# Performance work log

Hardware: AMD Instinct MI355X
Metric: run time of the kernel (lower is better)

## Reference

```python
import jax, jax.numpy as jnp
import numpy as np

L, B, S, D, H = 3, 2, 2048, 512, 8
HD = D // H
EPS = 1e-5
NEG = -1e9

def setup_inputs() -> dict:
    key = jax.random.key(0)
    ks = jax.random.split(key, 12)
    sc = 1.0 / np.sqrt(D)
    w = lambda k, shape: (jax.random.normal(k, shape, jnp.float32) * sc)
    return {
        'x': jax.random.normal(ks[0], (B, S, D), jnp.float32),
        'mask': jax.random.randint(ks[1], (B, S), 0, 2).astype(jnp.int32),
        'Wp': w(ks[2], (L, D, D)), 'bp': jnp.zeros((L, D), jnp.float32),
        'gamma': jnp.ones((L, D), jnp.float32), 'beta_ln': jnp.zeros((L, D), jnp.float32),
        'Wq': w(ks[3], (L, D, D)), 'bq': jnp.zeros((L, D), jnp.float32),
        'Wk': w(ks[4], (L, D, D)), 'bk': jnp.zeros((L, D), jnp.float32),
        'Wv': w(ks[5], (L, D, D)), 'bv': jnp.zeros((L, D), jnp.float32),
        'Wo': w(ks[6], (L, D, D)), 'bo': jnp.zeros((L, D), jnp.float32),
        'Wout': w(ks[7], (L * D, D)), 'bout': jnp.zeros((D,), jnp.float32),
    }

def reference(x, mask, Wp, bp, gamma, beta_ln, Wq, bq, Wk, bk, Wv, bv, Wo, bo, Wout, bout):
    # per-level input projection: [L,B,S,D]
    xl = jnp.einsum('bsd,lde->lbse', x, Wp) + bp[:, None, None, :]
    # LayerNorm over last dim
    m = xl.mean(-1, keepdims=True)
    v = xl.var(-1, keepdims=True)
    xn = (xl - m) / jnp.sqrt(v + EPS) * gamma[:, None, None, :] + beta_ln[:, None, None, :]
    proj = lambda W, b: (jnp.einsum('lbsd,lde->lbse', xn, W) + b[:, None, None, :]).reshape(L, B, S, H, HD)
    Q, K, V = proj(Wq, bq), proj(Wk, bk), proj(Wv, bv)
    scores = jnp.einsum('lbqhd,lbkhd->lbhqk', Q, K) / np.sqrt(HD).astype(np.float32)
    scores = jnp.where(mask[None, :, None, None, :] == 0, NEG, scores)
    attn = jax.nn.softmax(scores, axis=-1)  # dropout is identity in eval
    attended = jnp.einsum('lbhqk,lbkhd->lbqhd', attn, V).reshape(L, B, S, D)
    lev = jnp.einsum('lbsd,lde->lbse', attended, Wo) + bo[:, None, None, :]  # [L,B,S,D]
    combined = jnp.moveaxis(lev, 0, 2).reshape(B, S, L * D)  # concat levels on last dim
    return combined @ Wout + bout
```

## Files before the change

kernel.cpp:

```cpp
#include <hip/hip_runtime.h>

typedef unsigned short ushort_t;
typedef __attribute__((ext_vector_type(8))) short bf16x8;
typedef __attribute__((ext_vector_type(4))) float f32x4;
typedef __attribute__((ext_vector_type(4))) unsigned int u32x4;
typedef __attribute__((ext_vector_type(2))) unsigned int u32x2;

#define DI static __device__ __forceinline__

DI ushort_t f2bf(float f){
  unsigned u = __builtin_bit_cast(unsigned, f);
  u += 0x7fffu + ((u >> 16) & 1u);
  return (ushort_t)(u >> 16);
}
DI float bf2f(ushort_t h){ unsigned u = ((unsigned)h) << 16; return __builtin_bit_cast(float, u); }

DI unsigned cvt_pk_bf16(float a, float b){
  unsigned r;
  asm("v_cvt_pk_bf16_f32 %0, %1, %2" : "=v"(r) : "v"(a), "v"(b));
  return r;
}

DI float exp2_fast(float x){
  float r;
  asm("v_exp_f32 %0, %1" : "=v"(r) : "v"(x));
  return r;
}

DI void gload_lds16(const void* g, void* l){
  __builtin_amdgcn_global_load_lds((const __attribute__((address_space(1))) void*)g,
                                   (__attribute__((address_space(3))) void*)l, 16, 0, 0);
}

#define CLOG2E 0.18033688011112042f


__global__ __launch_bounds__(256)
void prep_kernel(const float* __restrict__ x, const float* __restrict__ Wo,
                 const float* __restrict__ Wp, const float* __restrict__ Wq,
                 const float* __restrict__ Wk, const float* __restrict__ Wv,
                 const float* __restrict__ Wout,
                 const float* __restrict__ bq, const float* __restrict__ bk,
                 const float* __restrict__ bv, const int* __restrict__ mask,
                 const float* __restrict__ bo, const float* __restrict__ bout,
                 ushort_t* __restrict__ xb, ushort_t* __restrict__ WoB,
                 ushort_t* __restrict__ WpT, ushort_t* __restrict__ WqkvT,
                 ushort_t* __restrict__ WoutT, float* __restrict__ bqkv,
                 ushort_t* __restrict__ mones, ushort_t* __restrict__ mzero,
                 float* __restrict__ zbias, float* __restrict__ bcomb){
  __shared__ float tile[32][33];
  const int bid = blockIdx.x, tid = threadIdx.x;

  auto do_cast = [&](const float* in, ushort_t* out, int i, int n4){
    if (i >= n4) return;
    float4 v = ((const float4*)in)[i];
    ushort_t r0 = f2bf(v.x), r1 = f2bf(v.y), r2 = f2bf(v.z), r3 = f2bf(v.w);
    ushort_t* o = out + (size_t)i * 4;
    o[0] = r0; o[1] = r1; o[2] = r2; o[3] = r3;
  };
  auto do_transpose = [&](const float* src, ushort_t* dst, int R, int C,
                          int bx, int by, float scale){
    int c0 = bx * 32, r0 = by * 32;
    int tx = tid & 31, ty = tid >> 5;
    #pragma unroll
    for (int p = 0; p < 4; ++p)
      tile[ty + p * 8][tx] = src[(size_t)(r0 + ty + p * 8) * C + c0 + tx];
    __syncthreads();
    #pragma unroll
    for (int p = 0; p < 4; ++p){
      int rr = ty + p * 8;
      dst[(size_t)(c0 + rr) * R + r0 + tx] = f2bf(tile[tx][rr] * scale);
    }
  };

  if (bid < 2048){
    do_cast(x, xb, bid * 256 + tid, 524288);
  } else if (bid < 2816){
    do_cast(Wo, WoB, (bid - 2048) * 256 + tid, 196608);
  } else if (bid < 5888){
    int idx = bid - 2816;
    int w = idx / 768, r = idx % 768;
    int zz = r >> 8, t = r & 255;
    int bx = t & 15, by = t >> 4;
    if (w == 0)      do_transpose(Wp + zz * 262144, WpT + zz * 262144, 512, 512, bx, by, 1.0f);
    else if (w == 1) do_transpose(Wq + zz * 262144, WqkvT + (size_t)zz * 786432, 512, 512, bx, by, CLOG2E);
    else if (w == 2) do_transpose(Wk + zz * 262144, WqkvT + 262144 + (size_t)zz * 786432, 512, 512, bx, by, 1.0f);
    else             do_transpose(Wv + zz * 262144, WqkvT + 524288 + (size_t)zz * 786432, 512, 512, bx, by, 1.0f);
  } else if (bid < 6656){
    int t = bid - 5888;
    do_transpose(Wout, WoutT, 1536, 512, t & 15, t >> 4, 1.0f);
  } else if (bid < 6674){
    int i = (bid - 6656) * 256 + tid;
    if (i < 4608){
      int l = i / 1536, j = i % 1536;
      float v = (j < 512) ? bq[l * 512 + j] * CLOG2E
              : (j < 1024 ? bk[l * 512 + j - 512] : bv[l * 512 + j - 1024]);
      bqkv[i] = v;
    }
  } else if (bid < 6690){
    int i = (bid - 6674) * 256 + tid;
    if (i < 4096){
      int mv = mask[i];
      mones[i] = mv ? (ushort_t)0x3F80 : (ushort_t)0;
      mzero[i] = mv ? (ushort_t)0xFFFF : (ushort_t)0;
    }
    if (i < 512) zbias[i] = 0.f;
  } else {
    int wid = tid >> 6, lane = tid & 63;
    int n = (bid - 6690) * 4 + wid;
    float s = 0.f;
    #pragma unroll
    for (int it = 0; it < 24; ++it){
      int k = it * 64 + lane;
      s += bo[k] * Wout[(size_t)k * 512 + n];
    }
    #pragma unroll
    for (int off = 32; off; off >>= 1) s += __shfl_xor(s, off);
    if (lane == 0) bcomb[n] = s + bout[n];
  }
}


template<int BN>
DI void gemm_mainloop(ushort_t* __restrict__ smem,
                      const ushort_t* __restrict__ A, const ushort_t* __restrict__ Bt,
                      int K, int lda, int ldb, int n0, int m0,
                      f32x4 (&acc)[4][BN / 32]){
  constexpr int NB = BN / 32;
  ushort_t* const As = smem;
  ushort_t* const Bs = smem + 128 * 64;
  const int tid = threadIdx.x, wid = tid >> 6, lane = tid & 63;
  const int wr = wid >> 1, wc = wid & 1, lr = lane & 15, lk = lane >> 4;

  for (int k0 = 0; k0 < K; k0 += 64){
    #pragma unroll
    for (int i = 0; i < 4; ++i){
      const int chunk = i * 256 + wid * 64 + lane;
      const int row = chunk >> 3, cc = chunk & 7;
      gload_lds16(A + (size_t)(m0 + row) * lda + (k0 + cc * 8), &As[(i * 256 + wid * 64) * 8]);
    }
    #pragma unroll
    for (int i = 0; i < NB; ++i){
      const int chunk = i * 256 + wid * 64 + lane;
      const int row = chunk >> 3, cc = chunk & 7;
      gload_lds16(Bt + (size_t)(n0 + row) * ldb + (k0 + cc * 8), &Bs[(i * 256 + wid * 64) * 8]);
    }
    __syncthreads();
    bf16x8 af[4][2], bfr[NB][2];
    #pragma unroll
    for (int m = 0; m < 4; ++m){
      af[m][0] = *(const bf16x8*)&As[(wr * 64 + m * 16 + lr) * 64 + lk * 8];
      af[m][1] = *(const bf16x8*)&As[(wr * 64 + m * 16 + lr) * 64 + 32 + lk * 8];
    }
    #pragma unroll
    for (int n = 0; n < NB; ++n){
      bfr[n][0] = *(const bf16x8*)&Bs[(wc * (BN / 2) + n * 16 + lr) * 64 + lk * 8];
      bfr[n][1] = *(const bf16x8*)&Bs[(wc * (BN / 2) + n * 16 + lr) * 64 + 32 + lk * 8];
    }
    #pragma unroll
    for (int m = 0; m < 4; ++m)
      #pragma unroll
      for (int n = 0; n < NB; ++n){
        acc[m][n] = __builtin_amdgcn_mfma_f32_16x16x32_bf16(af[m][0], bfr[n][0], acc[m][n], 0, 0, 0);
        acc[m][n] = __builtin_amdgcn_mfma_f32_16x16x32_bf16(af[m][1], bfr[n][1], acc[m][n], 0, 0, 0);
      }
    __syncthreads();
  }
}

template<int BF16OUT, int BN>
DI void gemm_store(const f32x4 (&acc)[4][BN / 32], const float* __restrict__ bias,
                   void* __restrict__ Cv, int n0, int m0, int ldc){
  constexpr int NB = BN / 32;
  const int tid = threadIdx.x, wid = tid >> 6, lane = tid & 63;
  const int wr = wid >> 1, wc = wid & 1, lr = lane & 15, lk = lane >> 4;
  #pragma unroll
  for (int n = 0; n < NB; ++n){
    const int col = n0 + wc * (BN / 2) + n * 16 + lr;
    const float bv = bias[col];
    #pragma unroll
    for (int m = 0; m < 4; ++m){
      const int row0 = m0 + wr * 64 + m * 16 + lk * 4;
      #pragma unroll
      for (int j = 0; j < 4; ++j){
        const float v = acc[m][n][j] + bv;
        const size_t idx = (size_t)(row0 + j) * ldc + col;
        if (BF16OUT) ((ushort_t*)Cv)[idx] = f2bf(v);
        else         ((float*)Cv)[idx] = v;
      }
    }
  }
}


template<int BF16OUT, int BN, int VT>
__global__ __launch_bounds__(256)
void gemm_bt(const ushort_t* __restrict__ A, const ushort_t* __restrict__ Bt,
             const float* __restrict__ bias, void* __restrict__ Cv,
             int M, int N, int K, int lda, int ldb, int ldc,
             long long sA, long long sB, long long sC, long long sBias,
             ushort_t* __restrict__ VtG, const ushort_t* __restrict__ mzero){
  constexpr int NB = BN / 32;
  __shared__ ushort_t smem[128 * 64 + BN * 64];
  const int z = blockIdx.z;
  A += (size_t)z * sA; Bt += (size_t)z * sB; bias += (size_t)z * sBias;
  const int n0 = blockIdx.x * BN, m0 = blockIdx.y * 128;
  const int tid = threadIdx.x, wid = tid >> 6, lane = tid & 63;
  const int wr = wid >> 1, wc = wid & 1, lr = lane & 15, lk = lane >> 4;

  f32x4 acc[4][NB] = {};
  gemm_mainloop<BN>(smem, A, Bt, K, lda, ldb, n0, m0, acc);

  if (VT && n0 >= 1024){
    #pragma unroll
    for (int n = 0; n < NB; ++n){
      const int c = wc * (BN / 2) + n * 16 + lr;
      const float bv = bias[n0 + c];
      #pragma unroll
      for (int m = 0; m < 4; ++m){
        const int r0 = wr * 64 + m * 16 + lk * 4;
        u32x2 pk;
        pk[0] = cvt_pk_bf16(acc[m][n][0] + bv, acc[m][n][1] + bv);
        pk[1] = cvt_pk_bf16(acc[m][n][2] + bv, acc[m][n][3] + bv);
        *(u32x2*)&smem[c * 128 + (r0 ^ ((c & 7) << 3))] = pk;
      }
    }
    __syncthreads();
    const int d_ = tid >> 1;
    const int gcol = n0 + d_;
    const int hh = (gcol - 1024) >> 6, dd = gcol & 63;
    const int b_ = m0 >> 11, s0g = m0 & 2047;
    ushort_t* dst = VtG + (((size_t)(z * 2 + b_) * 8 + hh) * 64 + dd) * 2048 + s0g;
    const ushort_t* mz = mzero + b_ * 2048 + s0g;
    #pragma unroll
    for (int it = 0; it < 8; ++it){
      const int s0 = (tid & 1) * 64 + it * 8;
      bf16x8 v = *(const bf16x8*)&smem[d_ * 128 + (s0 ^ ((d_ & 7) << 3))];
      const bf16x8 mzv = *(const bf16x8*)&mz[s0];
      v = v & mzv;
      *(bf16x8*)&dst[s0] = v;
    }
    return;
  }

  void* Cz = BF16OUT ? (void*)((ushort_t*)Cv + (size_t)z * sC)
                     : (void*)((float*)Cv + (size_t)z * sC);
  gemm_store<BF16OUT, BN>(acc, bias, Cz, n0, m0, ldc);
}

__global__ __launch_bounds__(256)
void gemm_dual(const ushort_t* __restrict__ WoutT, const ushort_t* __restrict__ WoB,
               const float* __restrict__ zbias, ushort_t* __restrict__ WcombT,
               const ushort_t* __restrict__ xb, const ushort_t* __restrict__ WpT,
               const float* __restrict__ bp, float* __restrict__ xl){
  __shared__ ushort_t smem[128 * 64 + 64 * 64];
  const int bid = blockIdx.x;
  f32x4 acc[4][2] = {};
  if (bid < 96){
    const int bx = bid & 7, by = (bid >> 3) & 3, z = bid >> 5;
    gemm_mainloop<64>(smem, WoutT + z * 512, WoB + (size_t)z * 262144,
                      512, 1536, 512, bx * 64, by * 128, acc);
    gemm_store<1, 64>(acc, zbias, WcombT + (size_t)z * 512, bx * 64, by * 128, 1536);
  } else {
    const int b2 = bid - 96;
    const int bx = b2 % 24, by = b2 / 24;
    gemm_mainloop<64>(smem, xb, WpT, 512, 512, 512, bx * 64, by * 128, acc);
    gemm_store<0, 64>(acc, bp, xl, bx * 64, by * 128, 1536);
  }
}


__global__ __launch_bounds__(256)
void ln_kernel(const float* __restrict__ xl, ushort_t* __restrict__ xn,
               const float* __restrict__ gamma, const float* __restrict__ beta){
  int rid = blockIdx.x * 4 + (threadIdx.x >> 6);
  int lane = threadIdx.x & 63;
  int l = rid >> 12, bs = rid & 4095;
  const float* row = xl + (size_t)bs * 1536 + l * 512;
  ushort_t* orow = xn + (size_t)bs * 1536 + l * 512;
  float4 a = ((const float4*)row)[lane * 2];
  float4 b4 = ((const float4*)row)[lane * 2 + 1];
  float vals[8] = {a.x, a.y, a.z, a.w, b4.x, b4.y, b4.z, b4.w};
  float s = 0.f, ss = 0.f;
  #pragma unroll
  for (int j = 0; j < 8; ++j){ s += vals[j]; ss += vals[j] * vals[j]; }
  #pragma unroll
  for (int off = 32; off; off >>= 1){
    s += __shfl_xor(s, off);
    ss += __shfl_xor(ss, off);
  }
  float mean = s * (1.0f / 512.0f);
  float var = ss * (1.0f / 512.0f) - mean * mean;
  float inv = rsqrtf(var + 1e-5f);
  const float* g = gamma + l * 512 + lane * 8;
  const float* be = beta + l * 512 + lane * 8;
  float4 g0 = ((const float4*)g)[0], g1 = ((const float4*)g)[1];
  float4 be0 = ((const float4*)be)[0], be1 = ((const float4*)be)[1];
  float gs[8] = {g0.x, g0.y, g0.z, g0.w, g1.x, g1.y, g1.z, g1.w};
  float bs8[8] = {be0.x, be0.y, be0.z, be0.w, be1.x, be1.y, be1.z, be1.w};
  bf16x8 r;
  #pragma unroll
  for (int j = 0; j < 8; ++j)
    r[j] = (short)f2bf((vals[j] - mean) * inv * gs[j] + bs8[j]);
  *(bf16x8*)(orow + lane * 8) = r;
}


__global__ __launch_bounds__(256)
void attn_kernel(const ushort_t* __restrict__ qkv, const ushort_t* __restrict__ VtG,
                 const ushort_t* __restrict__ mones, ushort_t* __restrict__ att){
  const int hz = blockIdx.x, qb = blockIdx.y;
  const int h = hz & 7, z = hz >> 3;
  const int l = z >> 1, b = z & 1;
  const size_t base = ((size_t)(l * 4096 + b * 2048)) * 1536;
  const ushort_t* Qb = qkv + base + h * 64;
  const ushort_t* Kb = qkv + base + 512 + h * 64;
  const ushort_t* Vt = VtG + ((size_t)(z * 8 + h) * 64) * 2048;

  __shared__ __attribute__((aligned(16))) ushort_t Ks[2][64 * 64];
  __shared__ __attribute__((aligned(16))) ushort_t Vs[2][64 * 64];

  const int tid = threadIdx.x, wid = tid >> 6, lane = tid & 63;
  const int lr = lane & 15, lk = lane >> 4;
  const int sw = lr & 7;
  const int qrow = qb * 64 + wid * 16 + lr;

  const ushort_t* qp = Qb + (size_t)qrow * 1536 + lk * 8;
  const bf16x8 q0 = *(const bf16x8*)qp;
  const bf16x8 q1 = *(const bf16x8*)(qp + 32);

  const int ch0 = wid * 64 + lane, ch1 = 256 + wid * 64 + lane;
  const int r0_ = ch0 >> 3, c0_ = (ch0 & 7) ^ (r0_ & 7);
  const int r1_ = ch1 >> 3, c1_ = (ch1 & 7) ^ (r1_ & 7);
  const ushort_t* kg0 = Kb + (size_t)r0_ * 1536 + c0_ * 8;
  const ushort_t* kg1 = Kb + (size_t)r1_ * 1536 + c1_ * 8;
  const ushort_t* vg0 = Vt + (size_t)r0_ * 2048 + c0_ * 8;
  const ushort_t* vg1 = Vt + (size_t)r1_ * 2048 + c1_ * 8;
  ushort_t* const kdA0 = &Ks[0][(wid * 64) * 8];
  ushort_t* const kdA1 = &Ks[0][(256 + wid * 64) * 8];
  ushort_t* const kdB0 = &Ks[1][(wid * 64) * 8];
  ushort_t* const kdB1 = &Ks[1][(256 + wid * 64) * 8];
  ushort_t* const vdA0 = &Vs[0][(wid * 64) * 8];
  ushort_t* const vdA1 = &Vs[0][(256 + wid * 64) * 8];
  ushort_t* const vdB0 = &Vs[1][(wid * 64) * 8];
  ushort_t* const vdB1 = &Vs[1][(256 + wid * 64) * 8];

  const ushort_t* const kbA0 = &Ks[0][lr * 64 + (lk ^ sw) * 8];
  const ushort_t* const kbA4 = &Ks[0][lr * 64 + ((lk ^ sw) ^ 4) * 8];
  const ushort_t* const kbB0 = &Ks[1][lr * 64 + (lk ^ sw) * 8];
  const ushort_t* const kbB4 = &Ks[1][lr * 64 + ((lk ^ sw) ^ 4) * 8];
  const ushort_t* const vbA0 = &Vs[0][lr * 64 + (lk ^ sw) * 8];
  const ushort_t* const vbA4 = &Vs[0][lr * 64 + ((lk ^ sw) ^ 4) * 8];
  const ushort_t* const vbB0 = &Vs[1][lr * 64 + (lk ^ sw) * 8];
  const ushort_t* const vbB4 = &Vs[1][lr * 64 + ((lk ^ sw) ^ 4) * 8];

  const ushort_t* pm = mones + b * 2048 + lk * 8;

  f32x4 o[4] = {};
  f32x4 lrun = {0.f, 0.f, 0.f, 0.f};

  gload_lds16(kg0, kdA0); gload_lds16(kg1, kdA1);
  gload_lds16(vg0, vdA0); gload_lds16(vg1, vdA1);
  kg0 += 98304; kg1 += 98304; vg0 += 64; vg1 += 64;
  __syncthreads();

  auto tile_step = [&](const ushort_t* kb0, const ushort_t* kb4,
                       const ushort_t* vb0, const ushort_t* vb4,
                       ushort_t* sk0, ushort_t* sk1, ushort_t* sv0, ushort_t* sv1,
                       bool doStage){
    if (doStage){
      gload_lds16(kg0, sk0); gload_lds16(kg1, sk1);
      gload_lds16(vg0, sv0); gload_lds16(vg1, sv1);
      kg0 += 98304; kg1 += 98304; vg0 += 64; vg1 += 64;
    }
    const bf16x8 mo0 = *(const bf16x8*)pm;
    const bf16x8 mo1 = *(const bf16x8*)(pm + 32);
    pm += 64;

    f32x4 t[4];
    __builtin_amdgcn_s_setprio(1);
    #pragma unroll
    for (int hh = 0; hh < 4; ++hh){
      const bf16x8 kf0 = *(const bf16x8*)(kb0 + hh * 1024);
      const bf16x8 kf1 = *(const bf16x8*)(kb4 + hh * 1024);
      f32x4 tt = {0.f, 0.f, 0.f, 0.f};
      tt = __builtin_amdgcn_mfma_f32_16x16x32_bf16(kf0, q0, tt, 0, 0, 0);
      tt = __builtin_amdgcn_mfma_f32_16x16x32_bf16(kf1, q1, tt, 0, 0, 0);
      t[hh] = tt;
    }
    __builtin_amdgcn_s_setprio(0);

    unsigned a00, a01, a10, a11, a20, a21, a30, a31;
    a00 = cvt_pk_bf16(exp2_fast(t[0][0]), exp2_fast(t[0][1]));
    a01 = cvt_pk_bf16(exp2_fast(t[0][2]), exp2_fast(t[0][3]));
    a10 = cvt_pk_bf16(exp2_fast(t[1][0]), exp2_fast(t[1][1]));
    a11 = cvt_pk_bf16(exp2_fast(t[1][2]), exp2_fast(t[1][3]));
    a20 = cvt_pk_bf16(exp2_fast(t[2][0]), exp2_fast(t[2][1]));
    a21 = cvt_pk_bf16(exp2_fast(t[2][2]), exp2_fast(t[2][3]));
    a30 = cvt_pk_bf16(exp2_fast(t[3][0]), exp2_fast(t[3][1]));
    a31 = cvt_pk_bf16(exp2_fast(t[3][2]), exp2_fast(t[3][3]));
    asm("v_permlane32_swap_b32 %0, %1" : "+v"(a00), "+v"(a10));
    asm("v_permlane32_swap_b32 %0, %1" : "+v"(a01), "+v"(a11));
    asm("v_permlane32_swap_b32 %0, %1" : "+v"(a20), "+v"(a30));
    asm("v_permlane32_swap_b32 %0, %1" : "+v"(a21), "+v"(a31));
    asm("v_permlane16_swap_b32 %0, %1" : "+v"(a00), "+v"(a10));
    asm("v_permlane16_swap_b32 %0, %1" : "+v"(a01), "+v"(a11));
    asm("v_permlane16_swap_b32 %0, %1" : "+v"(a20), "+v"(a30));
    asm("v_permlane16_swap_b32 %0, %1" : "+v"(a21), "+v"(a31));
    const u32x4 f0 = {a00, a01, a10, a11};
    const u32x4 f1 = {a20, a21, a30, a31};
    const bf16x8 pf0 = __builtin_bit_cast(bf16x8, f0);
    const bf16x8 pf1 = __builtin_bit_cast(bf16x8, f1);

    __builtin_amdgcn_s_setprio(1);
    lrun = __builtin_amdgcn_mfma_f32_16x16x32_bf16(pf0, mo0, lrun, 0, 0, 0);
    lrun = __builtin_amdgcn_mfma_f32_16x16x32_bf16(pf1, mo1, lrun, 0, 0, 0);
    #pragma unroll
    for (int n = 0; n < 4; ++n){
      const bf16x8 v0 = *(const bf16x8*)(vb0 + n * 1024);
      const bf16x8 v1 = *(const bf16x8*)(vb4 + n * 1024);
      o[n] = __builtin_amdgcn_mfma_f32_16x16x32_bf16(pf0, v0, o[n], 0, 0, 0);
      o[n] = __builtin_amdgcn_mfma_f32_16x16x32_bf16(pf1, v1, o[n], 0, 0, 0);
    }
    __builtin_amdgcn_s_setprio(0);
    __syncthreads();
  };

  for (int kt2 = 0; kt2 < 32; kt2 += 2){
    tile_step(kbA0, kbA4, vbA0, vbA4, kdB0, kdB1, vdB0, vdB1, true);
    tile_step(kbB0, kbB4, vbB0, vbB4, kdA0, kdA1, vdA0, vdA1, kt2 + 2 < 32);
  }

  float invj[4];
  #pragma unroll
  for (int j = 0; j < 4; ++j) invj[j] = 1.0f / lrun[j];
  const size_t arow0 = (size_t)(b * 2048 + qb * 64 + wid * 16);
  #pragma unroll
  for (int n = 0; n < 4; ++n)
    #pragma unroll
    for (int j = 0; j < 4; ++j)
      att[(arow0 + lk * 4 + j) * 1536 + l * 512 + h * 64 + n * 16 + lr] = f2bf(o[n][j] * invj[j]);
}


extern "C" void kernel_launch(void* const* d_in, const int* in_sizes, int n_in,
                              void* d_out, int out_size, void* d_ws, size_t ws_size,
                              hipStream_t stream){
  const float* x    = (const float*)d_in[0];
  const int*   mask = (const int*)d_in[1];
  const float* Wp   = (const float*)d_in[2];
  const float* bp   = (const float*)d_in[3];
  const float* gamma= (const float*)d_in[4];
  const float* beta = (const float*)d_in[5];
  const float* Wq   = (const float*)d_in[6];
  const float* bq   = (const float*)d_in[7];
  const float* Wk   = (const float*)d_in[8];
  const float* bk   = (const float*)d_in[9];
  const float* Wv   = (const float*)d_in[10];
  const float* bv   = (const float*)d_in[11];
  const float* Wo   = (const float*)d_in[12];
  const float* bo   = (const float*)d_in[13];
  const float* Wout = (const float*)d_in[14];
  const float* bout = (const float*)d_in[15];

  char* ws = (char*)d_ws;
  size_t off = 0;
  auto alloc = [&](size_t bytes){ void* p = ws + off; off += (bytes + 255) & ~(size_t)255; return p; };
  ushort_t* xb    = (ushort_t*)alloc(4096ull * 512 * 2);
  ushort_t* WpT   = (ushort_t*)alloc(1536ull * 512 * 2);
  ushort_t* WqkvT = (ushort_t*)alloc(3ull * 1536 * 512 * 2);
  ushort_t* WoB   = (ushort_t*)alloc(3ull * 512 * 512 * 2);
  ushort_t* WoutT = (ushort_t*)alloc(512ull * 1536 * 2);
  ushort_t* WcombT= (ushort_t*)alloc(512ull * 1536 * 2);
  float*    bqkv  = (float*)alloc(3ull * 1536 * 4);
  float*    zbias = (float*)alloc(512ull * 4);
  float*    bcomb = (float*)alloc(512ull * 4);
  ushort_t* monesB= (ushort_t*)alloc(4096ull * 2);
  ushort_t* mzeroB= (ushort_t*)alloc(4096ull * 2);
  float*    xl    = (float*)alloc(4096ull * 1536 * 4);
  ushort_t* xn    = (ushort_t*)alloc(4096ull * 1536 * 2);
  ushort_t* qkv   = (ushort_t*)alloc(3ull * 4096 * 1536 * 2);
  ushort_t* att   = (ushort_t*)xl;
  ushort_t* VtG   = (ushort_t*)((char*)xl + 12582912);

  prep_kernel<<<6818, 256, 0, stream>>>(x, Wo, Wp, Wq, Wk, Wv, Wout, bq, bk, bv,
                                        mask, bo, bout,
                                        xb, WoB, WpT, WqkvT, WoutT, bqkv,
                                        monesB, mzeroB, zbias, bcomb);

  gemm_dual<<<864, 256, 0, stream>>>(WoutT, WoB, zbias, WcombT, xb, WpT, bp, xl);

  ln_kernel<<<3072, 256, 0, stream>>>(xl, xn, gamma, beta);
  gemm_bt<1, 128, 1><<<dim3(12, 32, 3), 256, 0, stream>>>(xn, WqkvT, bqkv, qkv,
      4096, 1536, 512, 1536, 512, 1536, 512, 786432, 4096ll * 1536, 1536, VtG, mzeroB);
  attn_kernel<<<dim3(48, 32, 1), 256, 0, stream>>>(qkv, VtG, monesB, att);
  gemm_bt<0, 32, 0><<<dim3(16, 32, 1), 256, 0, stream>>>(att, WcombT, bcomb, (float*)d_out,
      4096, 512, 1536, 1536, 1536, 512, 0, 0, 0, 0, nullptr, nullptr);
}
```

Measured before the change: 189.1 us.

## Single-buffer V in attention and swizzle GEMM workgroup order

The attention kernel drops V double-buffering. It loads the next V tile into one shared buffer after the PV MFMAs and adds a barrier mid-step, so the V load overlaps the next tile's QK and softmax work. Shared memory per block shrinks, which could raise occupancy, but each step now has an extra barrier and V latency is less hidden. Separately, the GEMM kernels remap the flat workgroup id with a stride-8 permutation, likely to spread neighbouring tiles across XCDs for better L2 locality.

```diff
diff --git a/kernel.cpp b/kernel.cpp
--- a/kernel.cpp
+++ b/kernel.cpp
@@ -202,9 +202,16 @@
              ushort_t* __restrict__ VtG, const ushort_t* __restrict__ mzero){
   constexpr int NB = BN / 32;
   __shared__ ushort_t smem[128 * 64 + BN * 64];
-  const int z = blockIdx.z;
+  const int gx = gridDim.x, gy = gridDim.y;
+  const int nwg = gx * gy * gridDim.z;
+  int flat = blockIdx.x + gx * (blockIdx.y + gy * blockIdx.z);
+  flat = (flat & 7) * (nwg >> 3) + (flat >> 3);
+  const int bxi = flat % gx;
+  const int byi = (flat / gx) % gy;
+  const int z   = flat / (gx * gy);
+
   A += (size_t)z * sA; Bt += (size_t)z * sB; bias += (size_t)z * sBias;
-  const int n0 = blockIdx.x * BN, m0 = blockIdx.y * 128;
+  const int n0 = bxi * BN, m0 = byi * 128;
   const int tid = threadIdx.x, wid = tid >> 6, lane = tid & 63;
   const int wr = wid >> 1, wc = wid & 1, lr = lane & 15, lk = lane >> 4;
 
@@ -262,7 +269,8 @@
                       512, 1536, 512, bx * 64, by * 128, acc);
     gemm_store<1, 64>(acc, zbias, WcombT + (size_t)z * 512, bx * 64, by * 128, 1536);
   } else {
-    const int b2 = bid - 96;
+    int b2 = bid - 96;
+    b2 = (b2 & 7) * 96 + (b2 >> 3);
     const int bx = b2 % 24, by = b2 / 24;
     gemm_mainloop<64>(smem, xb, WpT, 512, 512, 512, bx * 64, by * 128, acc);
     gemm_store<0, 64>(acc, bp, xl, bx * 64, by * 128, 1536);
@@ -318,7 +326,7 @@
   const ushort_t* Vt = VtG + ((size_t)(z * 8 + h) * 64) * 2048;
 
   __shared__ __attribute__((aligned(16))) ushort_t Ks[2][64 * 64];
-  __shared__ __attribute__((aligned(16))) ushort_t Vs[2][64 * 64];
+  __shared__ __attribute__((aligned(16))) ushort_t Vs[64 * 64];
 
   const int tid = threadIdx.x, wid = tid >> 6, lane = tid & 63;
   const int lr = lane & 15, lk = lane >> 4;
@@ -340,19 +348,15 @@
   ushort_t* const kdA1 = &Ks[0][(256 + wid * 64) * 8];
   ushort_t* const kdB0 = &Ks[1][(wid * 64) * 8];
   ushort_t* const kdB1 = &Ks[1][(256 + wid * 64) * 8];
-  ushort_t* const vdA0 = &Vs[0][(wid * 64) * 8];
-  ushort_t* const vdA1 = &Vs[0][(256 + wid * 64) * 8];
-  ushort_t* const vdB0 = &Vs[1][(wid * 64) * 8];
-  ushort_t* const vdB1 = &Vs[1][(256 + wid * 64) * 8];
+  ushort_t* const vd0  = &Vs[(wid * 64) * 8];
+  ushort_t* const vd1  = &Vs[(256 + wid * 64) * 8];
 
   const ushort_t* const kbA0 = &Ks[0][lr * 64 + (lk ^ sw) * 8];
   const ushort_t* const kbA4 = &Ks[0][lr * 64 + ((lk ^ sw) ^ 4) * 8];
   const ushort_t* const kbB0 = &Ks[1][lr * 64 + (lk ^ sw) * 8];
   const ushort_t* const kbB4 = &Ks[1][lr * 64 + ((lk ^ sw) ^ 4) * 8];
-  const ushort_t* const vbA0 = &Vs[0][lr * 64 + (lk ^ sw) * 8];
-  const ushort_t* const vbA4 = &Vs[0][lr * 64 + ((lk ^ sw) ^ 4) * 8];
-  const ushort_t* const vbB0 = &Vs[1][lr * 64 + (lk ^ sw) * 8];
-  const ushort_t* const vbB4 = &Vs[1][lr * 64 + ((lk ^ sw) ^ 4) * 8];
+  const ushort_t* const vb0  = &Vs[lr * 64 + (lk ^ sw) * 8];
+  const ushort_t* const vb4  = &Vs[lr * 64 + ((lk ^ sw) ^ 4) * 8];
 
   const ushort_t* pm = mones + b * 2048 + lk * 8;
 
@@ -360,18 +364,15 @@
   f32x4 lrun = {0.f, 0.f, 0.f, 0.f};
 
   gload_lds16(kg0, kdA0); gload_lds16(kg1, kdA1);
-  gload_lds16(vg0, vdA0); gload_lds16(vg1, vdA1);
+  gload_lds16(vg0, vd0);  gload_lds16(vg1, vd1);
   kg0 += 98304; kg1 += 98304; vg0 += 64; vg1 += 64;
   __syncthreads();
 
   auto tile_step = [&](const ushort_t* kb0, const ushort_t* kb4,
-                       const ushort_t* vb0, const ushort_t* vb4,
-                       ushort_t* sk0, ushort_t* sk1, ushort_t* sv0, ushort_t* sv1,
-                       bool doStage){
-    if (doStage){
+                       ushort_t* sk0, ushort_t* sk1, bool stageK, bool stageV){
+    if (stageK){
       gload_lds16(kg0, sk0); gload_lds16(kg1, sk1);
-      gload_lds16(vg0, sv0); gload_lds16(vg1, sv1);
-      kg0 += 98304; kg1 += 98304; vg0 += 64; vg1 += 64;
+      kg0 += 98304; kg1 += 98304;
     }
     const bf16x8 mo0 = *(const bf16x8*)pm;
     const bf16x8 mo1 = *(const bf16x8*)(pm + 32);
@@ -412,6 +413,8 @@
     const bf16x8 pf0 = __builtin_bit_cast(bf16x8, f0);
     const bf16x8 pf1 = __builtin_bit_cast(bf16x8, f1);
 
+    __syncthreads();
+
     __builtin_amdgcn_s_setprio(1);
     lrun = __builtin_amdgcn_mfma_f32_16x16x32_bf16(pf0, mo0, lrun, 0, 0, 0);
     lrun = __builtin_amdgcn_mfma_f32_16x16x32_bf16(pf1, mo1, lrun, 0, 0, 0);
@@ -423,12 +426,17 @@
       o[n] = __builtin_amdgcn_mfma_f32_16x16x32_bf16(pf1, v1, o[n], 0, 0, 0);
     }
     __builtin_amdgcn_s_setprio(0);
-    __syncthreads();
+
+    if (stageV){
+      __syncthreads();
+      gload_lds16(vg0, vd0); gload_lds16(vg1, vd1);
+      vg0 += 64; vg1 += 64;
+    }
   };
 
   for (int kt2 = 0; kt2 < 32; kt2 += 2){
-    tile_step(kbA0, kbA4, vbA0, vbA4, kdB0, kdB1, vdB0, vdB1, true);
-    tile_step(kbB0, kbB4, vbB0, vbB4, kdA0, kdA1, vdA0, vdA1, kt2 + 2 < 32);
+    tile_step(kbA0, kbA4, kdB0, kdB1, true, true);
+    tile_step(kbB0, kbB4, kdA0, kdA1, kt2 + 2 < 32, kt2 + 2 < 32);
   }
 
   float invj[4];
```

Result: no change. 191.7 us (+1.4%).
